# Kernel optimization log

Measured on AMD Instinct MI355X. Metric: run time of the kernel, lower is better.

## Reference

```python
import jax, jax.numpy as jnp
import numpy as np

B, N, H = 8, 1024, 768
NH, HD = 12, 64  # num heads, head size
E = 131072       # total edges (avg degree 16)
N_REL = 30


def setup_inputs() -> dict:
    key = jax.random.key(0)
    ks = jax.random.split(key, 8)
    node_states = jax.random.normal(ks[0], (B, N, H), dtype=jnp.float32)
    eb = jax.random.randint(ks[1], (E,), 0, B, dtype=jnp.int32)
    ei = jax.random.randint(ks[2], (E,), 0, N, dtype=jnp.int32)
    ej = jax.random.randint(ks[3], (E,), 0, N, dtype=jnp.int32)
    er = jax.random.randint(ks[4], (E,), 0, N_REL, dtype=jnp.int32)
    edge_indices = jnp.stack([eb, ei, ej, er], axis=0)  # (4, E)
    scale = 1.0 / np.sqrt(H)
    Wq = jax.random.normal(ks[5], (H, H), dtype=jnp.float32) * scale
    Wk = jax.random.normal(ks[6], (H, H), dtype=jnp.float32) * scale
    Wv = jax.random.normal(ks[7], (H, H), dtype=jnp.float32) * scale
    return {"node_states": node_states, "edge_indices": edge_indices,
            "Wq": Wq, "Wk": Wk, "Wv": Wv}


def reference(node_states, edge_indices, Wq, Wk, Wv):
    # node_states: (B, N, H); edge_indices: (4, E) rows = (batch, head_node, tail_node, relation)
    b, i, j = edge_indices[0], edge_indices[1], edge_indices[2]
    q = (node_states @ Wq).reshape(B, N, NH, HD)
    k = (node_states @ Wk).reshape(B, N, NH, HD)
    v = (node_states @ Wv).reshape(B, N, NH, HD)
    qe = q[b, i]  # (E, NH, HD) gather at head nodes
    ke = k[b, j]  # (E, NH, HD) gather at tail nodes
    scores = jnp.einsum('ehd,ehd->eh', qe, ke) * (1.0 / np.sqrt(HD))  # (E, NH)
    seg = b * N + i  # segment = (batch, head_node)
    nseg = B * N
    smax = jax.ops.segment_max(scores, seg, num_segments=nseg)  # (nseg, NH)
    ex = jnp.exp(scores - smax[seg])
    denom = jax.ops.segment_sum(ex, seg, num_segments=nseg)
    probs = ex / jnp.maximum(denom[seg], 1e-9)  # (E, NH) edge softmax over tail nodes
    ve = v[b, j]  # (E, NH, HD)
    out_e = (probs[:, :, None] * ve).reshape(E, NH * HD)
    out = jax.ops.segment_sum(out_e, seg, num_segments=nseg)  # sum over tail dim
    return out.reshape(B, N, H)
```

## Files before the change

### kernel.cpp

```cpp
#include <hip/hip_runtime.h>
#include <hip/hip_fp16.h>

#define BB 8
#define NN 1024
#define HH 768
#define NHEAD 12
#define HD 64
#define NSEG 8192
#define QKVN 2304
#define MAXDEG 64

typedef unsigned short u16;
typedef __attribute__((ext_vector_type(8))) _Float16 f16x8;
typedef __attribute__((ext_vector_type(4))) float f32x4;
typedef __attribute__((ext_vector_type(4))) unsigned int u32x4;
typedef __attribute__((ext_vector_type(2))) unsigned int u32x2;

__device__ __forceinline__ u16 f2h(float f) {
  _Float16 h = (_Float16)f;
  return __builtin_bit_cast(u16, h);
}
__device__ __forceinline__ __half2 h2(unsigned int w) {
  return __builtin_bit_cast(__half2, w);
}

#define CAST_BLKS (NSEG * HH / 4 / 256)
#define TW_BLKS   ((QKVN / 32) * (HH / 32))
#define BUILD_BLKS 512

__global__ void prep_kernel(const float* __restrict__ X, u16* __restrict__ Xb,
                            const float* __restrict__ Wq, const float* __restrict__ Wk,
                            const float* __restrict__ Wv, u16* __restrict__ Wt,
                            const int* __restrict__ EI, int* __restrict__ cursor,
                            int* __restrict__ tailrow, int E) {
  const int bid = blockIdx.x;
  if (bid < CAST_BLKS) {
    int i = bid * 256 + threadIdx.x;
    float4 f = ((const float4*)X)[i];
    ushort4 o;
    o.x = f2h(f.x); o.y = f2h(f.y); o.z = f2h(f.z); o.w = f2h(f.w);
    ((ushort4*)Xb)[i] = o;
  } else if (bid < CAST_BLKS + TW_BLKS) {
    __shared__ float tile[32][33];
    int t = bid - CAST_BLKS;
    int n0 = (t % (QKVN / 32)) * 32;
    int k0 = (t / (QKVN / 32)) * 32;
    const float* W = (n0 < HH) ? Wq : (n0 < 2 * HH ? Wk : Wv);
    int nb = n0 - (n0 < HH ? 0 : (n0 < 2 * HH ? HH : 2 * HH));
    int tx = threadIdx.x & 31, ty = threadIdx.x >> 5;
#pragma unroll
    for (int r = 0; r < 4; ++r)
      tile[ty + 8 * r][tx] = W[(k0 + ty + 8 * r) * HH + nb + tx];
    __syncthreads();
#pragma unroll
    for (int r = 0; r < 4; ++r)
      Wt[(n0 + ty + 8 * r) * HH + k0 + tx] = f2h(tile[tx][ty + 8 * r]);
  } else {
    int e = (bid - CAST_BLKS - TW_BLKS) * 256 + threadIdx.x;
    if (e >= E) return;
    int b = EI[e];
    int seg = b * NN + EI[E + e];
    int j = EI[2 * E + e];
    int pos = atomicAdd(&cursor[seg], 1);
    if (pos < MAXDEG) tailrow[seg * MAXDEG + pos] = b * NN + j;
  }
}

#define GBM 256
#define GBN 128
#define GBK 32
#define GNT (HH / GBK)

__global__ __launch_bounds__(256, 2) void gemm_kernel(const u16* __restrict__ Xb,
                                                      const u16* __restrict__ Wt,
                                                      u16* __restrict__ QKV) {
  __shared__ u16 As[3][GBM * GBK];
  __shared__ u16 Bs[3][GBN * GBK];
  const int tid = threadIdx.x;
  const int wave = tid >> 6;
  const int lane = tid & 63;
  const int quad = lane >> 4;
  const int l15 = lane & 15;
  const int wm = (wave >> 1) * 128;
  const int wn = (wave & 1) * 64;

  const int bid = blockIdx.x;
  const int wgid = (bid & 7) * 72 + (bid >> 3);
  const int mt = wgid / 18;
  const int nt = wgid % 18;
  const int m0 = mt * GBM;
  const int n0 = nt * GBN;

  f32x4 acc[8][4] = {};

  auto stage_part = [&](int buf, int kt, int p) {
#pragma unroll
    for (int iss = 0; iss < 2; ++iss) {
      const int c = (p * 2 + iss) * 256 + tid;
      const int r = c >> 2;
      const u16* ga = Xb + (m0 + r) * HH + kt + (((c & 3) ^ (r & 3)) << 3);
      u16* la = &As[buf][c * 8];
      __builtin_amdgcn_global_load_lds(
          (const __attribute__((address_space(1))) unsigned int*)(unsigned long long)ga,
          (__attribute__((address_space(3))) unsigned int*)(unsigned long long)la, 16, 0, 0);
    }
    {
      const int c = p * 256 + tid;
      const int r = c >> 2;
      const u16* gb = Wt + (n0 + r) * HH + kt + (((c & 3) ^ (r & 3)) << 3);
      u16* lb = &Bs[buf][c * 8];
      __builtin_amdgcn_global_load_lds(
          (const __attribute__((address_space(1))) unsigned int*)(unsigned long long)gb,
          (__attribute__((address_space(3))) unsigned int*)(unsigned long long)lb, 16, 0, 0);
    }
  };

  stage_part(0, 0, 0);
  stage_part(0, 0, 1);
  stage_part(1, GBK, 0);
  stage_part(1, GBK, 1);

#pragma unroll 3
  for (int it = 0; it < GNT; ++it) {
    if (it != GNT - 1) {
      asm volatile("s_waitcnt vmcnt(6)" ::: "memory");
    } else {
      asm volatile("s_waitcnt vmcnt(0)" ::: "memory");
    }
    __builtin_amdgcn_s_barrier();
    const int b = it % 3;
    const int nb2 = (it + 2) % 3;
    const bool pre = (it + 2) < GNT;
    const int ktn = (it + 2) * GBK;

    f16x8 bfr[4];
#pragma unroll
    for (int s = 0; s < 2; ++s) {
      f16x8 afr[4];
#pragma unroll
      for (int mi = 0; mi < 4; ++mi) {
        const int m = wm + (s * 4 + mi) * 16 + l15;
        afr[mi] = *(const f16x8*)(&As[b][m * GBK + ((quad ^ (m & 3)) << 3)]);
      }
      if (s == 0) {
#pragma unroll
        for (int ni = 0; ni < 4; ++ni) {
          const int n = wn + ni * 16 + l15;
          bfr[ni] = *(const f16x8*)(&Bs[b][n * GBK + ((quad ^ (n & 3)) << 3)]);
        }
      }
      if (pre) stage_part(nb2, ktn, s);
      __builtin_amdgcn_s_barrier();
      asm volatile("s_waitcnt lgkmcnt(0)" ::: "memory");
      __builtin_amdgcn_sched_barrier(0);
      __builtin_amdgcn_s_setprio(1);
#pragma unroll
      for (int mi = 0; mi < 4; ++mi)
#pragma unroll
        for (int ni = 0; ni < 4; ++ni)
          acc[s * 4 + mi][ni] = __builtin_amdgcn_mfma_f32_16x16x32_f16(afr[mi], bfr[ni], acc[s * 4 + mi][ni], 0, 0, 0);
      __builtin_amdgcn_s_setprio(0);
    }
  }

#pragma unroll
  for (int mi = 0; mi < 8; ++mi)
#pragma unroll
    for (int ni = 0; ni < 4; ++ni) {
      const int col = n0 + wn + ni * 16 + l15;
#pragma unroll
      for (int r = 0; r < 4; ++r) {
        const int row = m0 + wm + mi * 16 + quad * 4 + r;
        QKV[row * QKVN + col] = f2h(acc[mi][ni][r]);
      }
    }
}

__global__ __launch_bounds__(256) void attn_kernel(const u16* __restrict__ QKV,
                                                   const int* __restrict__ tailrow,
                                                   const int* __restrict__ cursor,
                                                   float* __restrict__ out) {
  __shared__ float sm[3 * 16 * 64];
  const int wv = threadIdx.x >> 6;
  const int lane = threadIdx.x & 63;
  const int seg = (blockIdx.x & 7) * (NSEG / 8) + (blockIdx.x >> 3);
  const int base = seg * MAXDEG;
  int cnt = cursor[seg];
  if (cnt > MAXDEG) cnt = MAXDEG;
  const int myn = (cnt > wv) ? ((cnt - wv + 3) >> 2) : 0;

  int myidx = (lane < cnt) ? tailrow[base + lane] : 0;

  const u16* qrow = QKV + seg * QKVN;
  __half2 q1[4], q2[2];
  {
    u32x4 qa = *(const u32x4*)(qrow + lane * 8);
    u32x2 qb = *(const u32x2*)(qrow + 512 + lane * 4);
    const __half2 sc = __float2half2_rn(0.125f);
#pragma unroll
    for (int i = 0; i < 4; ++i) q1[i] = __hmul2(h2(qa[i]), sc);
    q2[0] = __hmul2(h2(qb[0]), sc);
    q2[1] = __hmul2(h2(qb[1]), sc);
  }

  float m1 = -__builtin_inff(), l1 = 0.f;
  float m2 = -__builtin_inff(), l2 = 0.f;
  __half2 o1[4] = {}, o2[2] = {};

  auto loadkv = [&](int row, u32x4& k1, u32x2& k2, u32x4& v1, u32x2& v2) {
    const u16* kp = QKV + row * QKVN + HH;
    k1 = *(const u32x4*)(kp + lane * 8);
    k2 = *(const u32x2*)(kp + 512 + lane * 4);
    v1 = *(const u32x4*)(kp + HH + lane * 8);
    v2 = *(const u32x2*)(kp + HH + 512 + lane * 4);
  };

  auto process = [&](u32x4 k1, u32x2 k2, u32x4 v1, u32x2 v2) {
    __half2 a1 = __hmul2(q1[0], h2(k1[0]));
    a1 = __hfma2(q1[1], h2(k1[1]), a1);
    a1 = __hfma2(q1[2], h2(k1[2]), a1);
    a1 = __hfma2(q1[3], h2(k1[3]), a1);
    float s1 = __low2float(a1) + __high2float(a1);
    s1 += __shfl_xor(s1, 1, 64);
    s1 += __shfl_xor(s1, 2, 64);
    s1 += __shfl_xor(s1, 4, 64);
    __half2 a2 = __hmul2(q2[0], h2(k2[0]));
    a2 = __hfma2(q2[1], h2(k2[1]), a2);
    float s2 = __low2float(a2) + __high2float(a2);
    s2 += __shfl_xor(s2, 1, 64);
    s2 += __shfl_xor(s2, 2, 64);
    s2 += __shfl_xor(s2, 4, 64);
    s2 += __shfl_xor(s2, 8, 64);
    {
      float mn = fmaxf(m1, s1);
      float al = __expf(m1 - mn);
      float ex = __expf(s1 - mn);
      l1 = l1 * al + ex;
      __half2 ah = __float2half2_rn(al), eh = __float2half2_rn(ex);
#pragma unroll
      for (int i = 0; i < 4; ++i)
        o1[i] = __hfma2(o1[i], ah, __hmul2(h2(v1[i]), eh));
      m1 = mn;
    }
    {
      float mn = fmaxf(m2, s2);
      float al = __expf(m2 - mn);
      float ex = __expf(s2 - mn);
      l2 = l2 * al + ex;
      __half2 ah = __float2half2_rn(al), eh = __float2half2_rn(ex);
      o2[0] = __hfma2(o2[0], ah, __hmul2(h2(v2[0]), eh));
      o2[1] = __hfma2(o2[1], ah, __hmul2(h2(v2[1]), eh));
      m2 = mn;
    }
  };

  if (myn > 0) {
    u32x4 k1c, v1c, k1n, v1n, k1n2, v1n2;
    u32x2 k2c, v2c, k2n, v2n, k2n2, v2n2;
    loadkv(__shfl(myidx, wv, 64), k1c, k2c, v1c, v2c);
    if (myn > 1) loadkv(__shfl(myidx, wv + 4, 64), k1n, k2n, v1n, v2n);
    for (int t = 0; t < myn; ++t) {
      if (t + 2 < myn)
        loadkv(__shfl(myidx, wv + 4 * (t + 2), 64), k1n2, k2n2, v1n2, v2n2);
      process(k1c, k2c, v1c, v2c);
      k1c = k1n; k2c = k2n; v1c = v1n; v2c = v2n;
      k1n = k1n2; k2n = k2n2; v1n = v1n2; v2n = v2n2;
    }
  }

  float of1[8], of2[4];
#pragma unroll
  for (int i = 0; i < 4; ++i) {
    of1[2 * i] = __low2float(o1[i]);
    of1[2 * i + 1] = __high2float(o1[i]);
  }
#pragma unroll
  for (int i = 0; i < 2; ++i) {
    of2[2 * i] = __low2float(o2[i]);
    of2[2 * i + 1] = __high2float(o2[i]);
  }

  if (wv > 0) {
    float* sb = sm + (wv - 1) * 1024;
    sb[0 * 64 + lane] = m1;  sb[1 * 64 + lane] = l1;
    sb[2 * 64 + lane] = m2;  sb[3 * 64 + lane] = l2;
#pragma unroll
    for (int i = 0; i < 8; ++i) sb[(4 + i) * 64 + lane] = of1[i];
#pragma unroll
    for (int i = 0; i < 4; ++i) sb[(12 + i) * 64 + lane] = of2[i];
  }
  __syncthreads();
  if (wv == 0) {
    float mn1 = fmaxf(m1, -1e30f), mn2 = fmaxf(m2, -1e30f);
#pragma unroll
    for (int j = 0; j < 3; ++j) {
      mn1 = fmaxf(mn1, sm[j * 1024 + 0 * 64 + lane]);
      mn2 = fmaxf(mn2, sm[j * 1024 + 2 * 64 + lane]);
    }
    float res1[8], res2[4];
    {
      float a0 = __expf(m1 - mn1);
      float l = l1 * a0;
#pragma unroll
      for (int i = 0; i < 8; ++i) res1[i] = of1[i] * a0;
#pragma unroll
      for (int j = 0; j < 3; ++j) {
        const float* sb = sm + j * 1024;
        float aj = __expf(sb[0 * 64 + lane] - mn1);
        l += sb[1 * 64 + lane] * aj;
#pragma unroll
        for (int i = 0; i < 8; ++i) res1[i] += sb[(4 + i) * 64 + lane] * aj;
      }
      float inv = 1.f / fmaxf(l, 1e-9f);
#pragma unroll
      for (int i = 0; i < 8; ++i) res1[i] *= inv;
    }
    {
      float a0 = __expf(m2 - mn2);
      float l = l2 * a0;
#pragma unroll
      for (int i = 0; i < 4; ++i) res2[i] = of2[i] * a0;
#pragma unroll
      for (int j = 0; j < 3; ++j) {
        const float* sb = sm + j * 1024;
        float aj = __expf(sb[2 * 64 + lane] - mn2);
        l += sb[3 * 64 + lane] * aj;
#pragma unroll
        for (int i = 0; i < 4; ++i) res2[i] += sb[(12 + i) * 64 + lane] * aj;
      }
      float inv = 1.f / fmaxf(l, 1e-9f);
#pragma unroll
      for (int i = 0; i < 4; ++i) res2[i] *= inv;
    }

    float* op = out + seg * HH;
    float4 r0 = {res1[0], res1[1], res1[2], res1[3]};
    float4 r1 = {res1[4], res1[5], res1[6], res1[7]};
    float4 r2 = {res2[0], res2[1], res2[2], res2[3]};
    ((float4*)(op + lane * 8))[0] = r0;
    ((float4*)(op + lane * 8))[1] = r1;
    *(float4*)(op + 512 + lane * 4) = r2;
  }
}

extern "C" void kernel_launch(void* const* d_in, const int* in_sizes, int n_in,
                              void* d_out, int out_size, void* d_ws, size_t ws_size,
                              hipStream_t stream) {
  const float* X  = (const float*)d_in[0];
  const int*   EI = (const int*)d_in[1];
  const float* Wq = (const float*)d_in[2];
  const float* Wk = (const float*)d_in[3];
  const float* Wv = (const float*)d_in[4];
  float* out = (float*)d_out;
  const int E = in_sizes[1] / 4;

  char* ws = (char*)d_ws;
  int* cursor  = (int*)(ws);
  int* tailrow = (int*)(ws + 32768);
  u16* Xb      = (u16*)(ws + 2129920);
  u16* Wt      = (u16*)(ws + 14712832);
  u16* QKV     = (u16*)(ws + 18251776);

  hipMemsetAsync(cursor, 0, NSEG * 4, stream);
  prep_kernel<<<CAST_BLKS + TW_BLKS + BUILD_BLKS, 256, 0, stream>>>(
      X, Xb, Wq, Wk, Wv, Wt, EI, cursor, tailrow, E);
  gemm_kernel<<<(NSEG / GBM) * (QKVN / GBN), 256, 0, stream>>>(Xb, Wt, QKV);
  attn_kernel<<<NSEG, 256, 0, stream>>>(QKV, tailrow, cursor, out);
}
```

Measured before the change: 165.8 us.

## Enlarge QKV GEMM tile to 256x256 with 512 threads and BK=64 double buffering

The QKV projection GEMM moves from 256x128 tiles with 4 waves and a triple-buffered BK=32 pipeline to 256x256 tiles with 8 waves and a double-buffered BK=64 pipeline. The LDS swizzle widens from 4 to 8 chunks. B-tile prefetch loads are interleaved between the MFMA sub-steps. The goal is more data reuse per block and fewer barriers per K step. The trade-off is that the 128KB LDS footprint likely allows only one block per CU, and 288 blocks on the CU count may leave a poorly balanced tail.

```diff
diff --git a/kernel.cpp b/kernel.cpp
--- a/kernel.cpp
+++ b/kernel.cpp
@@ -66,101 +66,101 @@
   }
 }
 
-#define GBM 256
-#define GBN 128
-#define GBK 32
-#define GNT (HH / GBK)
-
-__global__ __launch_bounds__(256, 2) void gemm_kernel(const u16* __restrict__ Xb,
+#define BM 256
+#define BN 256
+#define BKT 64
+#define NKT (HH / BKT)
+
+__global__ __launch_bounds__(512, 2) void gemm_kernel(const u16* __restrict__ Xb,
                                                       const u16* __restrict__ Wt,
                                                       u16* __restrict__ QKV) {
-  __shared__ u16 As[3][GBM * GBK];
-  __shared__ u16 Bs[3][GBN * GBK];
+  __shared__ u16 lds[2][2][BM * BKT];
   const int tid = threadIdx.x;
   const int wave = tid >> 6;
   const int lane = tid & 63;
   const int quad = lane >> 4;
   const int l15 = lane & 15;
-  const int wm = (wave >> 1) * 128;
-  const int wn = (wave & 1) * 64;
+  const int wm = (wave >> 2) * 128;
+  const int wn = (wave & 3) * 64;
 
   const int bid = blockIdx.x;
-  const int wgid = (bid & 7) * 72 + (bid >> 3);
-  const int mt = wgid / 18;
-  const int nt = wgid % 18;
-  const int m0 = mt * GBM;
-  const int n0 = nt * GBN;
+  const int wgid = (bid & 7) * 36 + (bid >> 3);
+  const int mt = wgid / 9;
+  const int nt = wgid % 9;
+  const int m0 = mt * BM;
+  const int n0 = nt * BN;
 
   f32x4 acc[8][4] = {};
 
-  auto stage_part = [&](int buf, int kt, int p) {
-#pragma unroll
-    for (int iss = 0; iss < 2; ++iss) {
-      const int c = (p * 2 + iss) * 256 + tid;
-      const int r = c >> 2;
-      const u16* ga = Xb + (m0 + r) * HH + kt + (((c & 3) ^ (r & 3)) << 3);
-      u16* la = &As[buf][c * 8];
+  auto stage_ht = [&](int kt, int ab, int hrow) {
+    const int buf = kt & 1;
+    const u16* src = ab ? (Wt + n0 * HH) : (Xb + m0 * HH);
+#pragma unroll
+    for (int ld = 0; ld < 2; ++ld) {
+      const int cl = ld * 512 + tid;
+      const int r = hrow * 128 + (cl >> 3);
+      const int p = cl & 7;
+      const int lg = p ^ (r & 7);
+      const u16* g = src + r * HH + kt * BKT + lg * 8;
+      u16* l = &lds[buf][ab][r * 64 + p * 8];
       __builtin_amdgcn_global_load_lds(
-          (const __attribute__((address_space(1))) unsigned int*)(unsigned long long)ga,
-          (__attribute__((address_space(3))) unsigned int*)(unsigned long long)la, 16, 0, 0);
-    }
-    {
-      const int c = p * 256 + tid;
-      const int r = c >> 2;
-      const u16* gb = Wt + (n0 + r) * HH + kt + (((c & 3) ^ (r & 3)) << 3);
-      u16* lb = &Bs[buf][c * 8];
-      __builtin_amdgcn_global_load_lds(
-          (const __attribute__((address_space(1))) unsigned int*)(unsigned long long)gb,
-          (__attribute__((address_space(3))) unsigned int*)(unsigned long long)lb, 16, 0, 0);
+          (const __attribute__((address_space(1))) unsigned int*)(unsigned long long)g,
+          (__attribute__((address_space(3))) unsigned int*)(unsigned long long)l, 16, 0, 0);
     }
   };
 
-  stage_part(0, 0, 0);
-  stage_part(0, 0, 1);
-  stage_part(1, GBK, 0);
-  stage_part(1, GBK, 1);
-
-#pragma unroll 3
-  for (int it = 0; it < GNT; ++it) {
-    if (it != GNT - 1) {
-      asm volatile("s_waitcnt vmcnt(6)" ::: "memory");
+  stage_ht(0, 0, 0); stage_ht(0, 0, 1); stage_ht(0, 1, 0); stage_ht(0, 1, 1);
+
+  f16x8 bfr[4];
+
+#pragma unroll 2
+  for (int kt = 0; kt < NKT; ++kt) {
+    const int buf = kt & 1;
+    const bool pre = (kt + 1) < NKT;
+
+    if (pre) {
+      stage_ht(kt + 1, 0, 0);
+      stage_ht(kt + 1, 0, 1);
+      asm volatile("s_waitcnt vmcnt(4)" ::: "memory");
     } else {
       asm volatile("s_waitcnt vmcnt(0)" ::: "memory");
     }
     __builtin_amdgcn_s_barrier();
-    const int b = it % 3;
-    const int nb2 = (it + 2) % 3;
-    const bool pre = (it + 2) < GNT;
-    const int ktn = (it + 2) * GBK;
-
-    f16x8 bfr[4];
-#pragma unroll
-    for (int s = 0; s < 2; ++s) {
-      f16x8 afr[4];
-#pragma unroll
-      for (int mi = 0; mi < 4; ++mi) {
-        const int m = wm + (s * 4 + mi) * 16 + l15;
-        afr[mi] = *(const f16x8*)(&As[b][m * GBK + ((quad ^ (m & 3)) << 3)]);
+
+#pragma unroll
+    for (int ks = 0; ks < 2; ++ks) {
+#pragma unroll
+      for (int mh = 0; mh < 2; ++mh) {
+        f16x8 afr[4];
+#pragma unroll
+        for (int mi = 0; mi < 4; ++mi) {
+          const int rr = wm + mh * 64 + mi * 16 + l15;
+          const int pp = (ks * 4 + quad) ^ (rr & 7);
+          afr[mi] = *(const f16x8*)(&lds[buf][0][rr * 64 + pp * 8]);
+        }
+        if (mh == 0) {
+#pragma unroll
+          for (int ni = 0; ni < 4; ++ni) {
+            const int rn = wn + ni * 16 + l15;
+            const int pp = (ks * 4 + quad) ^ (rn & 7);
+            bfr[ni] = *(const f16x8*)(&lds[buf][1][rn * 64 + pp * 8]);
+          }
+        }
+        if (pre && ks == 0 && mh == 1) stage_ht(kt + 1, 1, 0);
+        if (pre && ks == 1 && mh == 0) stage_ht(kt + 1, 1, 1);
+        asm volatile("s_waitcnt lgkmcnt(0)" ::: "memory");
+        __builtin_amdgcn_sched_barrier(0);
+        __builtin_amdgcn_s_setprio(1);
+#pragma unroll
+        for (int mi = 0; mi < 4; ++mi)
+#pragma unroll
+          for (int ni = 0; ni < 4; ++ni)
+            acc[mh * 4 + mi][ni] = __builtin_amdgcn_mfma_f32_16x16x32_f16(
+                afr[mi], bfr[ni], acc[mh * 4 + mi][ni], 0, 0, 0);
+        __builtin_amdgcn_s_setprio(0);
       }
-      if (s == 0) {
-#pragma unroll
-        for (int ni = 0; ni < 4; ++ni) {
-          const int n = wn + ni * 16 + l15;
-          bfr[ni] = *(const f16x8*)(&Bs[b][n * GBK + ((quad ^ (n & 3)) << 3)]);
-        }
-      }
-      if (pre) stage_part(nb2, ktn, s);
-      __builtin_amdgcn_s_barrier();
-      asm volatile("s_waitcnt lgkmcnt(0)" ::: "memory");
-      __builtin_amdgcn_sched_barrier(0);
-      __builtin_amdgcn_s_setprio(1);
-#pragma unroll
-      for (int mi = 0; mi < 4; ++mi)
-#pragma unroll
-        for (int ni = 0; ni < 4; ++ni)
-          acc[s * 4 + mi][ni] = __builtin_amdgcn_mfma_f32_16x16x32_f16(afr[mi], bfr[ni], acc[s * 4 + mi][ni], 0, 0, 0);
-      __builtin_amdgcn_s_setprio(0);
-    }
+    }
+    __builtin_amdgcn_s_barrier();
   }
 
 #pragma unroll
@@ -364,6 +364,6 @@
   hipMemsetAsync(cursor, 0, NSEG * 4, stream);
   prep_kernel<<<CAST_BLKS + TW_BLKS + BUILD_BLKS, 256, 0, stream>>>(
       X, Xb, Wq, Wk, Wv, Wt, EI, cursor, tailrow, E);
-  gemm_kernel<<<(NSEG / GBM) * (QKVN / GBN), 256, 0, stream>>>(Xb, Wt, QKV);
+  gemm_kernel<<<(NSEG / BM) * (QKVN / BN), 512, 0, stream>>>(Xb, Wt, QKV);
   attn_kernel<<<NSEG, 256, 0, stream>>>(QKV, tailrow, cursor, out);
 }
```

New measurement: 170.1 us. 2.6% more time.
